# Performance work log

Measured on AMD Instinct MI355X. Metric: run time of the kernel, lower is better.

The kernel has to match this reference:

```python
import jax, jax.numpy as jnp
import numpy as np
import math

B, IMG, P, C_IN = 32, 32, 2, 4
D, TED, L, H = 768, 256, 12, 12
GRID = IMG // P            # 16
N = GRID * GRID            # 256 patches
HD = D // H                # 64 head dim
MLP_H = 4 * D
RPD = 2 * GRID - 1         # 31 relative-position table side


def _ln(x, w, b, eps=1e-6):
    m = x.mean(-1, keepdims=True)
    v = ((x - m) ** 2).mean(-1, keepdims=True)
    return (x - m) * jax.lax.rsqrt(v + eps) * w + b


def _rel_idx():
    c = jnp.arange(GRID)
    ch, cw = jnp.meshgrid(c, c, indexing='ij')
    cf = jnp.stack([ch.reshape(-1), cw.reshape(-1)])          # [2, N]
    rel = cf[:, :, None] - cf[:, None, :] + (GRID - 1)        # [2, N, N] in [0, 2*GRID-2]
    return rel[0], rel[1]


def setup_inputs() -> dict:
    key = jax.random.key(0)
    ks = iter(jax.random.split(key, 64))
    def nrm(shape, s=0.02):
        return jax.random.normal(next(ks), shape, jnp.float32) * s
    z = lambda *s: jnp.zeros(s, jnp.float32)
    o = lambda *s: jnp.ones(s, jnp.float32)
    return dict(
        x=jax.random.normal(next(ks), (B, C_IN, IMG, IMG), jnp.float32),
        t=jax.random.uniform(next(ks), (B,), jnp.float32) * 1000.0,
        patch_w=nrm((D, C_IN, P, P), 0.5), patch_b=z(D),
        pos_embed=nrm((1, N, D)),
        t_w1=nrm((TED, D)), t_b1=z(D), t_w2=nrm((D, D)), t_b2=z(D),
        norm1_w=o(L, D), norm1_b=z(L, D),
        wqs=nrm((L, D, D)), bqs=z(L, D), wqt=nrm((L, D, D)), bqt=z(L, D),
        wks=nrm((L, D, D)), bks=z(L, D), wkt=nrm((L, D, D)), bkt=z(L, D),
        wvs=nrm((L, D, D)), bvs=z(L, D), wvt=nrm((L, D, D)), bvt=z(L, D),
        attn_proj_w=nrm((L, D, D)), attn_proj_b=z(L, D),
        rpb=nrm((L, RPD, RPD, H)),
        norm2_w=o(L, D), norm2_b=z(L, D),
        mlp_w1=nrm((L, D, MLP_H)), mlp_b1=z(L, MLP_H),
        mlp_w2=nrm((L, MLP_H, D)), mlp_b2=z(L, D),
        norm_w=o(D), norm_b=z(D),
        dec_w=nrm((D, P * P * C_IN)), dec_b=z(P * P * C_IN),
    )


def reference(x, t, patch_w, patch_b, pos_embed, t_w1, t_b1, t_w2, t_b2,
              norm1_w, norm1_b, wqs, bqs, wqt, bqt, wks, bks, wkt, bkt,
              wvs, bvs, wvt, bvt, attn_proj_w, attn_proj_b, rpb,
              norm2_w, norm2_b, mlp_w1, mlp_b1, mlp_w2, mlp_b2,
              norm_w, norm_b, dec_w, dec_b):
    Bn = x.shape[0]
    # patch embed: stride==kernel Conv2d as reshape + einsum -> [B, N, D]
    xr = x.reshape(Bn, C_IN, GRID, P, GRID, P)
    x_s = jnp.einsum('bcipjq,ecpq->bije', xr, patch_w).reshape(Bn, N, D) + patch_b
    x_s = x_s + pos_embed
    # sinusoidal time embedding + MLP -> [B, D]
    half = TED // 2
    freq = jnp.exp(jnp.arange(half, dtype=jnp.float32) * (-math.log(10000.0) / (half - 1)))
    emb = t[:, None] * freq[None, :]
    emb = jnp.concatenate([jnp.sin(emb), jnp.cos(emb)], axis=-1)
    x_t = jax.nn.silu(emb @ t_w1 + t_b1) @ t_w2 + t_b2
    ih, iw = _rel_idx()
    scale = HD ** -0.5
    for l in range(L):
        h = _ln(x_s, norm1_w[l], norm1_b[l])
        q = h @ wqs[l] + bqs[l] + (x_t @ wqt[l] + bqt[l])[:, None, :]
        k = h @ wks[l] + bks[l] + (x_t @ wkt[l] + bkt[l])[:, None, :]
        v = h @ wvs[l] + bvs[l] + (x_t @ wvt[l] + bvt[l])[:, None, :]
        q = q.reshape(Bn, N, H, HD)
        k = k.reshape(Bn, N, H, HD)
        v = v.reshape(Bn, N, H, HD)
        bias = rpb[l][ih, iw]                                  # gather: [N, N, H]
        attn = jnp.einsum('bnhd,bmhd->bhnm', q, k) * scale + bias.transpose(2, 0, 1)[None]
        attn = jax.nn.softmax(attn, axis=-1)
        o_ = jnp.einsum('bhnm,bmhd->bnhd', attn, v).reshape(Bn, N, D)
        x_s = x_s + (o_ @ attn_proj_w[l] + attn_proj_b[l])
        h2 = _ln(x_s, norm2_w[l], norm2_b[l])
        x_s = x_s + (jax.nn.silu(h2 @ mlp_w1[l] + mlp_b1[l]) @ mlp_w2[l] + mlp_b2[l])
    x_s = _ln(x_s, norm_w, norm_b)
    x_s = x_s @ dec_w + dec_b                                  # [B, N, P*P*C]
    # unpatchify -> [B, C, IMG, IMG]
    xo = x_s.reshape(Bn, GRID, GRID, C_IN, P, P).transpose(0, 3, 1, 4, 2, 5)
    return xo.reshape(Bn, C_IN, GRID * P, GRID * P)
```

## Files before the change

### kernel.cpp

```cpp
#include <hip/hip_runtime.h>
#include <hip/hip_bf16.h>

typedef __attribute__((ext_vector_type(8))) short short8;
typedef __attribute__((ext_vector_type(4))) short s16x4;
typedef __attribute__((ext_vector_type(4))) float f32x4;
typedef __hip_bfloat16 bf16;

#define AS1 __attribute__((address_space(1)))
#define AS3 __attribute__((address_space(3)))

__device__ __forceinline__ float b2f(short u) {
  union { unsigned int i; float f; } x;
  x.i = ((unsigned int)(unsigned short)u) << 16;
  return x.f;
}
__device__ __forceinline__ short f2bs(float f) {
  bf16 t = __float2bfloat16(f);
  return *reinterpret_cast<short*>(&t);
}

__device__ __forceinline__ void gld_lds16(const void* g, void* lds) {
  __builtin_amdgcn_global_load_lds((const AS1 unsigned int*)g,
                                   (AS3 unsigned int*)lds, 16, 0, 0);
}

__global__ void transpose_conv(const float* __restrict__ src, bf16* __restrict__ dst,
                               int R, int C, int row_off, long long layer_stride) {
  __shared__ float t[32][33];
  int l = blockIdx.z;
  int r0 = blockIdx.y * 32;
  int c0 = blockIdx.x * 32;
  int tx = threadIdx.x & 31, ty = threadIdx.x >> 5;
  const float* s = src + (size_t)l * R * C;
#pragma unroll
  for (int i = 0; i < 4; ++i)
    t[ty + i * 8][tx] = s[(size_t)(r0 + ty + i * 8) * C + c0 + tx];
  __syncthreads();
  bf16* d = dst + (size_t)l * layer_stride;
#pragma unroll
  for (int i = 0; i < 4; ++i) {
    int n = c0 + ty + i * 8, k = r0 + tx;
    d[(size_t)(row_off + n) * R + k] = __float2bfloat16(t[tx][ty + i * 8]);
  }
}

__global__ void dec_transpose(const float* __restrict__ dw, bf16* __restrict__ dwT) {
  int idx = blockIdx.x * 256 + threadIdx.x;
  if (idx >= 12288) return;
  int k = idx % 768, j = idx / 768;
  dwT[j * 768 + k] = __float2bfloat16(dw[k * 16 + j]);
}

__global__ void patch_embed(const float* __restrict__ x, const float* __restrict__ pw,
                            const float* __restrict__ pb, const float* __restrict__ pos,
                            float* __restrict__ xs) {
  int idx = blockIdx.x * 256 + threadIdx.x;
  int d = idx % 768;
  int n = (idx / 768) & 255;
  int b = idx / (768 * 256);
  int gi = n >> 4, gj = n & 15;
  float acc = pb[d];
#pragma unroll
  for (int c = 0; c < 4; ++c)
#pragma unroll
    for (int p = 0; p < 2; ++p)
#pragma unroll
      for (int q = 0; q < 2; ++q)
        acc += x[((b * 4 + c) * 32 + gi * 2 + p) * 32 + gj * 2 + q] *
               pw[((d * 4 + c) * 2 + p) * 2 + q];
  xs[idx] = acc + pos[n * 768 + d];
}

__global__ void temb_kernel(const float* __restrict__ t, float* __restrict__ emb) {
  int b = blockIdx.x;
  int i = threadIdx.x;
  float f = __expf((float)i * (-logf(10000.f) / 127.f));
  float e = t[b] * f;
  emb[b * 256 + i] = sinf(e);
  emb[b * 256 + 128 + i] = cosf(e);
}

template <int MODE>
__global__ void smallmm_red(const float* __restrict__ in, const float* __restrict__ w,
                            const float* __restrict__ bias, void* __restrict__ out, int K) {
  int tid = threadIdx.x;
  int s = tid & 7, o = blockIdx.x * 32 + (tid >> 3);
  int d = o % 768, b = o / 768;
  int Ks = K >> 3, k0 = s * Ks;
  const float* ir = in + b * K + k0;
  const float* wr = w + (size_t)k0 * 768 + d;
  float a = 0.f;
  for (int i = 0; i < Ks; ++i) a += ir[i] * wr[(size_t)i * 768];
  a += __shfl_xor(a, 1);
  a += __shfl_xor(a, 2);
  a += __shfl_xor(a, 4);
  if (s == 0) {
    a += bias[d];
    if (MODE == 0) {
      a = a / (1.f + __expf(-a));
      ((float*)out)[o] = a;
    } else {
      ((bf16*)out)[o] = __float2bfloat16(a);
    }
  }
}

__global__ void build_btab_frag(const float* __restrict__ rpb, bf16* __restrict__ btf) {
  int idx = blockIdx.x * 256 + threadIdx.x;
  int t = idx & 65535;
  int lh = idx >> 16;
  int h = lh % 12, l = lh / 12;
  int r = t & 3; t >>= 2;
  int lane = t & 63; t >>= 6;
  int i = t & 3; t >>= 2;
  int w = t & 3; t >>= 2;
  int jb = t & 1; t >>= 1;
  int hc = t & 7;
  int q = w * 64 + i * 16 + (lane & 15);
  int k = hc * 32 + jb * 16 + (lane >> 4) * 4 + r;
  int ih = (q >> 4) - (k >> 4) + 15;
  int iw = (q & 15) - (k & 15) + 15;
  btf[idx] = __float2bfloat16(8.0f * rpb[((l * 31 + ih) * 31 + iw) * 12 + h]);
}

__global__ __launch_bounds__(256) void ln_bf16_kernel(const float* __restrict__ x,
                                                      const float* __restrict__ w,
                                                      const float* __restrict__ b,
                                                      bf16* __restrict__ out) {
  int row = blockIdx.x;
  int tid = threadIdx.x;
  const float* xr = x + (size_t)row * 768;
  float v[3];
  float s = 0.f, s2 = 0.f;
#pragma unroll
  for (int i = 0; i < 3; ++i) {
    v[i] = xr[tid + i * 256];
    s += v[i];
    s2 += v[i] * v[i];
  }
#pragma unroll
  for (int off = 32; off; off >>= 1) {
    s += __shfl_down(s, off);
    s2 += __shfl_down(s2, off);
  }
  __shared__ float ps[4], ps2[4];
  int wid = tid >> 6, lane = tid & 63;
  if (lane == 0) { ps[wid] = s; ps2[wid] = s2; }
  __syncthreads();
  s = ps[0] + ps[1] + ps[2] + ps[3];
  s2 = ps2[0] + ps2[1] + ps2[2] + ps2[3];
  float m = s * (1.f / 768.f);
  float var = s2 * (1.f / 768.f) - m * m;
  float r = rsqrtf(var + 1e-6f);
#pragma unroll
  for (int i = 0; i < 3; ++i) {
    int c = tid + i * 256;
    out[(size_t)row * 768 + c] = __float2bfloat16((v[i] - m) * r * w[c] + b[c]);
  }
}

template <int EPI>
__global__ __launch_bounds__(256) void gemm128(
    const bf16* __restrict__ A, int lda, const bf16* __restrict__ BT, int ldb, int K,
    const float* __restrict__ p0, const float* __restrict__ p1,
    const float* __restrict__ p2, const float* __restrict__ p3,
    const float* __restrict__ p4, const float* __restrict__ p5,
    const float* __restrict__ resid, float* __restrict__ outF,
    bf16* __restrict__ outB, int ldc) {
  __shared__ __align__(16) char lds[65536];
  const int tid = threadIdx.x;
  const int wid = tid >> 6, lane = tid & 63;
  const int wr = wid >> 1, wc = wid & 1;
  const int nwg = gridDim.x * gridDim.y;
  const int bid = blockIdx.y * gridDim.x + blockIdx.x;
  const int swzb = (bid & 7) * (nwg >> 3) + (bid >> 3);
  const int m0 = (swzb / gridDim.x) * 128, n0 = (swzb % gridDim.x) * 128;
  const int l16 = lane & 15, lq = lane >> 4;

  f32x4 acc[4][4];
#pragma unroll
  for (int i = 0; i < 4; ++i)
#pragma unroll
    for (int j = 0; j < 4; ++j) acc[i][j] = f32x4{0.f, 0.f, 0.f, 0.f};

  const int arow = tid >> 3;
  const int aslot = (tid & 7) ^ (arow & 7);
  const bf16* gA = A + (size_t)(m0 + arow) * lda + aslot * 8;
  const bf16* gB = BT + (size_t)(n0 + arow) * ldb + aslot * 8;
  const unsigned offw = (unsigned)__builtin_amdgcn_readfirstlane((tid & ~63) * 16);

  const int NT = K >> 6;
  auto stage = [&](int buf, int t) {
    char* p = lds + buf * 32768;
    const int k = t * 64;
#pragma unroll
    for (int it = 0; it < 4; ++it) {
      gld_lds16(gA + (size_t)it * 32 * lda + k, p + it * 4096 + offw);
      gld_lds16(gB + (size_t)it * 32 * ldb + k, p + 16384 + it * 4096 + offw);
    }
  };

  stage(0, 0);
  const unsigned swb = ((unsigned)(l16 & 7)) << 4;
  for (int t = 0; t < NT; ++t) {
    char* cur = lds + (t & 1) * 32768;
    if (t + 1 < NT) {
      stage((t + 1) & 1, t + 1);
      asm volatile("s_waitcnt vmcnt(8)" ::: "memory");
    } else {
      asm volatile("s_waitcnt vmcnt(0)" ::: "memory");
    }
    __builtin_amdgcn_s_barrier();
#pragma unroll
    for (int ks = 0; ks < 2; ++ks) {
      short8 af[4], bfr[4];
      const unsigned ko = ((unsigned)(ks * 64 + lq * 16)) ^ swb;
#pragma unroll
      for (int i = 0; i < 4; ++i) {
        af[i]  = *(const short8*)(cur + (wr * 64 + i * 16 + l16) * 128 + ko);
        bfr[i] = *(const short8*)(cur + 16384 + (wc * 64 + i * 16 + l16) * 128 + ko);
      }
#pragma unroll
      for (int i = 0; i < 4; ++i)
#pragma unroll
        for (int j = 0; j < 4; ++j)
          acc[i][j] = __builtin_amdgcn_mfma_f32_16x16x32_bf16(af[i], bfr[j], acc[i][j], 0, 0, 0);
    }
    __builtin_amdgcn_s_barrier();
  }

#pragma unroll
  for (int i = 0; i < 4; ++i) {
#pragma unroll
    for (int j = 0; j < 4; ++j) {
#pragma unroll
      for (int r = 0; r < 4; ++r) {
        int row = m0 + wr * 64 + i * 16 + lq * 4 + r;
        int col = n0 + wc * 64 + j * 16 + l16;
        float v = acc[i][j][r];
        if constexpr (EPI == 0) {
          int s = col / 768, d = col % 768;
          int b = row >> 8;
          const float* bs = (s == 0) ? p0 : (s == 1) ? p1 : p2;
          const float* ts = (s == 0) ? p3 : (s == 1) ? p4 : p5;
          v += bs[d] + ts[b * 768 + d];
          outB[(size_t)row * ldc + col] = __float2bfloat16(v);
        } else if constexpr (EPI == 1) {
          v += p0[col] + resid[(size_t)row * ldc + col];
          outF[(size_t)row * ldc + col] = v;
        } else if constexpr (EPI == 2) {
          v += p0[col];
          v = v / (1.f + __expf(-v));
          outB[(size_t)row * ldc + col] = __float2bfloat16(v);
        } else if constexpr (EPI == 3) {
          if (row < 32) {
            int l = col / 2304;
            int r2c = col - l * 2304;
            int s = r2c / 768, d = r2c - s * 768;
            const float* bs = (s == 0) ? p0 : (s == 1) ? p1 : p2;
            v += bs[l * 768 + d];
            outF[(size_t)((l * 3 + s) * 32 + row) * 768 + d] = v;
          }
        } else {
          if (col < 16) {
            v += p0[col];
            int b = row >> 8, n = row & 255;
            int gi = n >> 4, gj = n & 15;
            int c = col >> 2, pp = (col >> 1) & 1, qq = col & 1;
            outF[((b * 4 + c) * 32 + gi * 2 + pp) * 32 + gj * 2 + qq] = v;
          }
        }
      }
    }
  }
}

__global__ __launch_bounds__(256) void attn_mfma(const bf16* __restrict__ qkv,
                                                 const bf16* __restrict__ btf,
                                                 bf16* __restrict__ obuf) {
  __shared__ __align__(16) char lds[65536];
  const int tid = threadIdx.x;
  const int wave = tid >> 6, lane = tid & 63;
  const int l16 = lane & 15, lq = lane >> 4;
  const int b = blockIdx.x / 12, h = blockIdx.x % 12;
  const bf16* qb = qkv + (size_t)b * 256 * 2304;

  {
    const short8* vrow = (const short8*)(qb + (size_t)tid * 2304 + 1536 + h * 64);
    short8 vv[8];
#pragma unroll
    for (int c = 0; c < 8; ++c) vv[c] = vrow[c];
#pragma unroll
    for (int c = 0; c < 8; ++c)
#pragma unroll
      for (int e = 0; e < 8; ++e) {
        int d = c * 8 + e;
        unsigned off = (unsigned)(d * 512 + tid * 2) ^ ((unsigned)(d & 7) << 4);
        *(short*)(lds + off) = vv[c][e];
      }
  }
  short8 qf[4][2];
#pragma unroll
  for (int i = 0; i < 4; ++i)
#pragma unroll
    for (int ks = 0; ks < 2; ++ks)
      qf[i][ks] = *(const short8*)(qb + (size_t)(wave * 64 + i * 16 + l16) * 2304 +
                                   h * 64 + ks * 32 + lq * 8);
  __syncthreads();

  f32x4 oacc[4][4];
#pragma unroll
  for (int i = 0; i < 4; ++i)
#pragma unroll
    for (int j = 0; j < 4; ++j) oacc[i][j] = f32x4{0.f, 0.f, 0.f, 0.f};
  float lp[4] = {0.f, 0.f, 0.f, 0.f};
  const bf16* bl = btf + (size_t)h * 65536 + lane * 4;
  const unsigned swzv = ((unsigned)(l16 & 7)) << 4;
  const unsigned swzp = ((unsigned)(l16 & 3)) << 4;

  for (int hc = 0; hc < 8; ++hc) {
    short8 kf[2][2];
#pragma unroll
    for (int jb = 0; jb < 2; ++jb) {
      const bf16* kr = qb + (size_t)(hc * 32 + jb * 16 + l16) * 2304 + 768 + h * 64 + lq * 8;
      kf[jb][0] = *(const short8*)(kr);
      kf[jb][1] = *(const short8*)(kr + 32);
    }
    f32x4 sacc[4][2];
#pragma unroll
    for (int i = 0; i < 4; ++i)
#pragma unroll
      for (int jb = 0; jb < 2; ++jb) {
        s16x4 bv = *(const s16x4*)(bl + ((size_t)((hc * 2 + jb) * 16 + wave * 4 + i) << 8));
        sacc[i][jb] = f32x4{b2f(bv[0]), b2f(bv[1]), b2f(bv[2]), b2f(bv[3])};
      }
#pragma unroll
    for (int jb = 0; jb < 2; ++jb)
#pragma unroll
      for (int i = 0; i < 4; ++i) {
        sacc[i][jb] = __builtin_amdgcn_mfma_f32_16x16x32_bf16(kf[jb][0], qf[i][0], sacc[i][jb], 0, 0, 0);
        sacc[i][jb] = __builtin_amdgcn_mfma_f32_16x16x32_bf16(kf[jb][1], qf[i][1], sacc[i][jb], 0, 0, 0);
      }
    char* Pw = lds + 32768 + (hc & 1) * 16384 + wave * 4096;
#pragma unroll
    for (int i = 0; i < 4; ++i)
#pragma unroll
      for (int jb = 0; jb < 2; ++jb) {
        float p0 = __expf(sacc[i][jb][0] * 0.125f);
        float p1 = __expf(sacc[i][jb][1] * 0.125f);
        float p2 = __expf(sacc[i][jb][2] * 0.125f);
        float p3 = __expf(sacc[i][jb][3] * 0.125f);
        lp[i] += (p0 + p1) + (p2 + p3);
        s16x4 pk = {f2bs(p0), f2bs(p1), f2bs(p2), f2bs(p3)};
        *(s16x4*)(Pw + (i * 16 + l16) * 64 + (((unsigned)(jb * 32 + lq * 8)) ^ swzp)) = pk;
      }
    asm volatile("s_waitcnt lgkmcnt(0)" ::: "memory");
    __builtin_amdgcn_sched_barrier(0);
    short8 pa[4], vb[4];
#pragma unroll
    for (int i = 0; i < 4; ++i)
      pa[i] = *(const short8*)(Pw + (i * 16 + l16) * 64 + (((unsigned)(lq * 16)) ^ swzp));
#pragma unroll
    for (int dj = 0; dj < 4; ++dj)
      vb[dj] = *(const short8*)(lds + (dj * 16 + l16) * 512 +
                                (((unsigned)(hc * 64 + lq * 16)) ^ swzv));
#pragma unroll
    for (int i = 0; i < 4; ++i)
#pragma unroll
      for (int dj = 0; dj < 4; ++dj)
        oacc[i][dj] = __builtin_amdgcn_mfma_f32_16x16x32_bf16(pa[i], vb[dj], oacc[i][dj], 0, 0, 0);
  }

#pragma unroll
  for (int i = 0; i < 4; ++i) {
    float l = lp[i];
    l += __shfl_xor(l, 16);
    l += __shfl_xor(l, 32);
#pragma unroll
    for (int r = 0; r < 4; ++r) {
      float linv = 1.f / __shfl(l, lq * 4 + r);
      int grow = b * 256 + wave * 64 + i * 16 + lq * 4 + r;
#pragma unroll
      for (int dj = 0; dj < 4; ++dj)
        obuf[(size_t)grow * 768 + h * 64 + dj * 16 + l16] =
            __float2bfloat16(oacc[i][dj][r] * linv);
    }
  }
}

extern "C" void kernel_launch(void* const* d_in, const int* in_sizes, int n_in,
                              void* d_out, int out_size, void* d_ws, size_t ws_size,
                              hipStream_t stream) {
  (void)in_sizes; (void)n_in; (void)out_size; (void)ws_size;
  const float* x       = (const float*)d_in[0];
  const float* t_in    = (const float*)d_in[1];
  const float* patch_w = (const float*)d_in[2];
  const float* patch_b = (const float*)d_in[3];
  const float* pos     = (const float*)d_in[4];
  const float* t_w1    = (const float*)d_in[5];
  const float* t_b1    = (const float*)d_in[6];
  const float* t_w2    = (const float*)d_in[7];
  const float* t_b2    = (const float*)d_in[8];
  const float* norm1_w = (const float*)d_in[9];
  const float* norm1_b = (const float*)d_in[10];
  const float* wqs     = (const float*)d_in[11];
  const float* bqs     = (const float*)d_in[12];
  const float* wqt     = (const float*)d_in[13];
  const float* bqt     = (const float*)d_in[14];
  const float* wks     = (const float*)d_in[15];
  const float* bks     = (const float*)d_in[16];
  const float* wkt     = (const float*)d_in[17];
  const float* bkt     = (const float*)d_in[18];
  const float* wvs     = (const float*)d_in[19];
  const float* bvs     = (const float*)d_in[20];
  const float* wvt     = (const float*)d_in[21];
  const float* bvt     = (const float*)d_in[22];
  const float* projw   = (const float*)d_in[23];
  const float* projb   = (const float*)d_in[24];
  const float* rpb     = (const float*)d_in[25];
  const float* norm2_w = (const float*)d_in[26];
  const float* norm2_b = (const float*)d_in[27];
  const float* mlp_w1  = (const float*)d_in[28];
  const float* mlp_b1  = (const float*)d_in[29];
  const float* mlp_w2  = (const float*)d_in[30];
  const float* mlp_b2  = (const float*)d_in[31];
  const float* norm_w  = (const float*)d_in[32];
  const float* norm_b  = (const float*)d_in[33];
  const float* dec_w   = (const float*)d_in[34];
  const float* dec_b   = (const float*)d_in[35];

  char* ws = (char*)d_ws;
  size_t off = 0;
  auto alloc = [&](size_t bytes) -> void* {
    void* p = ws + off;
    off += (bytes + 255) & ~(size_t)255;
    return p;
  };
  bf16* wqkvT = (bf16*)alloc(12ull * 2304 * 768 * 2);
  bf16* projT = (bf16*)alloc(12ull * 768 * 768 * 2);
  bf16* mlp1T = (bf16*)alloc(12ull * 3072 * 768 * 2);
  bf16* mlp2T = (bf16*)alloc(12ull * 768 * 3072 * 2);
  bf16* wtT   = (bf16*)alloc(12ull * 2304 * 768 * 2);
  float* xs   = (float*)alloc(8192ull * 768 * 4);
  bf16* hbuf  = (bf16*)alloc(8192ull * 768 * 2);
  bf16* qkvb  = (bf16*)alloc(8192ull * 2304 * 2);
  bf16* obuf  = (bf16*)alloc(8192ull * 768 * 2);
  bf16* btabf = (bf16*)alloc(12ull * 12 * 256 * 256 * 2);
  float* ttok = (float*)alloc(12ull * 3 * 32 * 768 * 4);
  bf16* xtb   = (bf16*)alloc(128ull * 768 * 2);
  bf16* dwT   = (bf16*)alloc(128ull * 768 * 2);
  float* emb  = (float*)alloc(32ull * 256 * 4);
  float* h1   = (float*)alloc(32ull * 768 * 4);
  bf16* hmlp  = qkvb;

  hipMemsetAsync(xtb, 0, 128ull * 768 * 2, stream);
  hipMemsetAsync(dwT, 0, 128ull * 768 * 2, stream);

  transpose_conv<<<dim3(24, 24, 12), 256, 0, stream>>>(wqs, wqkvT, 768, 768, 0, 2304ll * 768);
  transpose_conv<<<dim3(24, 24, 12), 256, 0, stream>>>(wks, wqkvT, 768, 768, 768, 2304ll * 768);
  transpose_conv<<<dim3(24, 24, 12), 256, 0, stream>>>(wvs, wqkvT, 768, 768, 1536, 2304ll * 768);
  transpose_conv<<<dim3(24, 24, 12), 256, 0, stream>>>(projw, projT, 768, 768, 0, 768ll * 768);
  transpose_conv<<<dim3(96, 24, 12), 256, 0, stream>>>(mlp_w1, mlp1T, 768, 3072, 0, 3072ll * 768);
  transpose_conv<<<dim3(24, 96, 12), 256, 0, stream>>>(mlp_w2, mlp2T, 3072, 768, 0, 768ll * 3072);
  transpose_conv<<<dim3(24, 24, 12), 256, 0, stream>>>(wqt, wtT, 768, 768, 0, 2304ll * 768);
  transpose_conv<<<dim3(24, 24, 12), 256, 0, stream>>>(wkt, wtT, 768, 768, 768, 2304ll * 768);
  transpose_conv<<<dim3(24, 24, 12), 256, 0, stream>>>(wvt, wtT, 768, 768, 1536, 2304ll * 768);
  dec_transpose<<<48, 256, 0, stream>>>(dec_w, dwT);
  build_btab_frag<<<36864, 256, 0, stream>>>(rpb, btabf);

  temb_kernel<<<32, 128, 0, stream>>>(t_in, emb);
  smallmm_red<0><<<768, 256, 0, stream>>>(emb, t_w1, t_b1, h1, 256);
  smallmm_red<1><<<768, 256, 0, stream>>>(h1, t_w2, t_b2, xtb, 768);
  gemm128<3><<<dim3(216, 1), 256, 0, stream>>>(
      xtb, 768, wtT, 768, 768, bqt, bkt, bvt, nullptr, nullptr, nullptr,
      nullptr, ttok, nullptr, 0);

  patch_embed<<<24576, 256, 0, stream>>>(x, patch_w, patch_b, pos, xs);

  for (int l = 0; l < 12; ++l) {
    ln_bf16_kernel<<<8192, 256, 0, stream>>>(xs, norm1_w + l * 768, norm1_b + l * 768, hbuf);
    gemm128<0><<<dim3(18, 64), 256, 0, stream>>>(
        hbuf, 768, wqkvT + (size_t)l * 2304 * 768, 768, 768,
        bqs + l * 768, bks + l * 768, bvs + l * 768,
        ttok + (size_t)(l * 3 + 0) * 32 * 768,
        ttok + (size_t)(l * 3 + 1) * 32 * 768,
        ttok + (size_t)(l * 3 + 2) * 32 * 768,
        nullptr, nullptr, qkvb, 2304);
    attn_mfma<<<384, 256, 0, stream>>>(qkvb, btabf + (size_t)l * 12 * 65536, obuf);
    gemm128<1><<<dim3(6, 64), 256, 0, stream>>>(
        obuf, 768, projT + (size_t)l * 768 * 768, 768, 768,
        projb + l * 768, nullptr, nullptr, nullptr, nullptr, nullptr,
        xs, xs, nullptr, 768);
    ln_bf16_kernel<<<8192, 256, 0, stream>>>(xs, norm2_w + l * 768, norm2_b + l * 768, hbuf);
    gemm128<2><<<dim3(24, 64), 256, 0, stream>>>(
        hbuf, 768, mlp1T + (size_t)l * 3072 * 768, 768, 768,
        mlp_b1 + l * 3072, nullptr, nullptr, nullptr, nullptr, nullptr,
        nullptr, nullptr, hmlp, 3072);
    gemm128<1><<<dim3(6, 64), 256, 0, stream>>>(
        hmlp, 3072, mlp2T + (size_t)l * 768 * 3072, 3072, 3072,
        mlp_b2 + l * 768, nullptr, nullptr, nullptr, nullptr, nullptr,
        xs, xs, nullptr, 768);
  }
  ln_bf16_kernel<<<8192, 256, 0, stream>>>(xs, norm_w, norm_b, hbuf);
  gemm128<4><<<dim3(1, 64), 256, 0, stream>>>(
      hbuf, 768, dwT, 768, 768, dec_b, nullptr, nullptr, nullptr, nullptr, nullptr,
      nullptr, (float*)d_out, nullptr, 0);
}
```

Baseline: 2.841 ms.

## Replace 128x128 GEMM with 256x128 tile, 8 waves, quadrant-phased pipeline

The GEMM tile grows from 128x128 with 4 waves to 256x128 with 8 waves, and LDS rises to 96 KB. The K-loop is split into four quadrant phases, each of which issues part of the next stages' global-to-LDS loads before its MFMA burst. MFMA runs are wrapped in raised s_setprio, and the block swizzle is made conditional on the grid size. The aim is more reuse of A/B per tile and better overlap of loads with MFMA, at the cost of one workgroup per CU and fewer workgroups for the narrow N=768 GEMMs. The xtb buffer is enlarged so the timestep GEMM can read 256 rows.

After: 3.314 ms. 16.6% more time.

```diff
diff --git a/kernel.cpp b/kernel.cpp
--- a/kernel.cpp
+++ b/kernel.cpp
@@ -159,23 +159,59 @@
   }
 }
 
+#define ENDB do { __builtin_amdgcn_sched_barrier(0); __builtin_amdgcn_s_barrier(); \
+                  __builtin_amdgcn_sched_barrier(0); } while (0)
+
+#define PH(MQ, NQ, STG) do {                                                         \
+    char* pa = lds + ((t & 1) << 15) + (MQ << 14);                                   \
+    char* pb = lds + 65536 + ((t & 1) << 14) + (NQ << 13);                           \
+    short8 af0, af1, af2, af3, bg0, bg1, bg2, bg3;                                   \
+    {                                                                                \
+      int ra0 = wm * 32 + l16, ra1 = ra0 + 16;                                       \
+      unsigned sa0 = (unsigned)(ra0 & 7) << 4, sa1 = (unsigned)(ra1 & 7) << 4;       \
+      af0 = *(const short8*)(pa + ra0 * 128 + (((unsigned)(lq * 16)) ^ sa0));        \
+      af1 = *(const short8*)(pa + ra0 * 128 + (((unsigned)(64 + lq * 16)) ^ sa0));   \
+      af2 = *(const short8*)(pa + ra1 * 128 + (((unsigned)(lq * 16)) ^ sa1));        \
+      af3 = *(const short8*)(pa + ra1 * 128 + (((unsigned)(64 + lq * 16)) ^ sa1));   \
+      int rb0 = wn * 32 + l16, rb1 = rb0 + 16;                                       \
+      unsigned sb0 = (unsigned)(rb0 & 7) << 4, sb1 = (unsigned)(rb1 & 7) << 4;       \
+      bg0 = *(const short8*)(pb + rb0 * 128 + (((unsigned)(lq * 16)) ^ sb0));        \
+      bg1 = *(const short8*)(pb + rb0 * 128 + (((unsigned)(64 + lq * 16)) ^ sb0));   \
+      bg2 = *(const short8*)(pb + rb1 * 128 + (((unsigned)(lq * 16)) ^ sb1));        \
+      bg3 = *(const short8*)(pb + rb1 * 128 + (((unsigned)(64 + lq * 16)) ^ sb1));   \
+    }                                                                                \
+    STG;                                                                             \
+    ENDB;                                                                            \
+    __builtin_amdgcn_s_setprio(1);                                                   \
+    acc[MQ*2+0][NQ*2+0] = __builtin_amdgcn_mfma_f32_16x16x32_bf16(af0, bg0, acc[MQ*2+0][NQ*2+0], 0, 0, 0); \
+    acc[MQ*2+0][NQ*2+0] = __builtin_amdgcn_mfma_f32_16x16x32_bf16(af1, bg1, acc[MQ*2+0][NQ*2+0], 0, 0, 0); \
+    acc[MQ*2+0][NQ*2+1] = __builtin_amdgcn_mfma_f32_16x16x32_bf16(af0, bg2, acc[MQ*2+0][NQ*2+1], 0, 0, 0); \
+    acc[MQ*2+0][NQ*2+1] = __builtin_amdgcn_mfma_f32_16x16x32_bf16(af1, bg3, acc[MQ*2+0][NQ*2+1], 0, 0, 0); \
+    acc[MQ*2+1][NQ*2+0] = __builtin_amdgcn_mfma_f32_16x16x32_bf16(af2, bg0, acc[MQ*2+1][NQ*2+0], 0, 0, 0); \
+    acc[MQ*2+1][NQ*2+0] = __builtin_amdgcn_mfma_f32_16x16x32_bf16(af3, bg1, acc[MQ*2+1][NQ*2+0], 0, 0, 0); \
+    acc[MQ*2+1][NQ*2+1] = __builtin_amdgcn_mfma_f32_16x16x32_bf16(af2, bg2, acc[MQ*2+1][NQ*2+1], 0, 0, 0); \
+    acc[MQ*2+1][NQ*2+1] = __builtin_amdgcn_mfma_f32_16x16x32_bf16(af3, bg3, acc[MQ*2+1][NQ*2+1], 0, 0, 0); \
+    __builtin_amdgcn_s_setprio(0);                                                   \
+  } while (0)
+
 template <int EPI>
-__global__ __launch_bounds__(256) void gemm128(
+__global__ __launch_bounds__(512, 1) void gemm256(
     const bf16* __restrict__ A, int lda, const bf16* __restrict__ BT, int ldb, int K,
     const float* __restrict__ p0, const float* __restrict__ p1,
     const float* __restrict__ p2, const float* __restrict__ p3,
     const float* __restrict__ p4, const float* __restrict__ p5,
     const float* __restrict__ resid, float* __restrict__ outF,
     bf16* __restrict__ outB, int ldc) {
-  __shared__ __align__(16) char lds[65536];
+  __shared__ __align__(16) char lds[98304];
   const int tid = threadIdx.x;
   const int wid = tid >> 6, lane = tid & 63;
-  const int wr = wid >> 1, wc = wid & 1;
+  const int wm = wid >> 1, wn = wid & 1;
+  const int l16 = lane & 15, lq = lane >> 4;
+
   const int nwg = gridDim.x * gridDim.y;
-  const int bid = blockIdx.y * gridDim.x + blockIdx.x;
-  const int swzb = (bid & 7) * (nwg >> 3) + (bid >> 3);
-  const int m0 = (swzb / gridDim.x) * 128, n0 = (swzb % gridDim.x) * 128;
-  const int l16 = lane & 15, lq = lane >> 4;
+  int bid = blockIdx.y * gridDim.x + blockIdx.x;
+  if (!(nwg & 7)) bid = (bid & 7) * (nwg >> 3) + (bid >> 3);
+  const int m0 = (bid / gridDim.x) * 256, n0 = (bid % gridDim.x) * 128;
 
   f32x4 acc[4][4];
 #pragma unroll
@@ -183,50 +219,44 @@
 #pragma unroll
     for (int j = 0; j < 4; ++j) acc[i][j] = f32x4{0.f, 0.f, 0.f, 0.f};
 
-  const int arow = tid >> 3;
-  const int aslot = (tid & 7) ^ (arow & 7);
-  const bf16* gA = A + (size_t)(m0 + arow) * lda + aslot * 8;
-  const bf16* gB = BT + (size_t)(n0 + arow) * ldb + aslot * 8;
+  const int u5 = (tid >> 3) & 31;
+  const int slot = (tid & 7) ^ ((tid >> 3) & 7);
+  const bf16* gA = A + (size_t)m0 * lda + slot * 8;
+  const bf16* gB = BT + (size_t)n0 * ldb + slot * 8;
   const unsigned offw = (unsigned)__builtin_amdgcn_readfirstlane((tid & ~63) * 16);
 
-  const int NT = K >> 6;
-  auto stage = [&](int buf, int t) {
-    char* p = lds + buf * 32768;
-    const int k = t * 64;
-#pragma unroll
-    for (int it = 0; it < 4; ++it) {
-      gld_lds16(gA + (size_t)it * 32 * lda + k, p + it * 4096 + offw);
-      gld_lds16(gB + (size_t)it * 32 * ldb + k, p + 16384 + it * 4096 + offw);
+  auto stageA = [&](int tt, int mq) {
+    char* dst = lds + ((tt & 1) << 15) + (mq << 14);
+#pragma unroll
+    for (int e = 0; e < 2; ++e) {
+      int srow = (e * 2 + (tid >> 8)) * 64 + mq * 32 + u5;
+      gld_lds16(gA + (size_t)srow * lda + tt * 64, dst + e * 8192 + offw);
     }
   };
-
-  stage(0, 0);
-  const unsigned swb = ((unsigned)(l16 & 7)) << 4;
+  auto stageB = [&](int tt, int nq) {
+    char* dst = lds + 65536 + ((tt & 1) << 14) + (nq << 13);
+    int srow = ((tid >> 8) & 1) * 64 + nq * 32 + u5;
+    gld_lds16(gB + (size_t)srow * ldb + tt * 64, dst + offw);
+  };
+
+  const int NT = K >> 6;
+  stageA(0, 0); stageA(0, 1); stageB(0, 0); stageB(0, 1);
+  stageB(1, 0); stageA(1, 0);
+  asm volatile("s_waitcnt vmcnt(3)" ::: "memory");
+  __builtin_amdgcn_s_barrier();
+  __builtin_amdgcn_sched_barrier(0);
+
   for (int t = 0; t < NT; ++t) {
-    char* cur = lds + (t & 1) * 32768;
-    if (t + 1 < NT) {
-      stage((t + 1) & 1, t + 1);
-      asm volatile("s_waitcnt vmcnt(8)" ::: "memory");
-    } else {
-      asm volatile("s_waitcnt vmcnt(0)" ::: "memory");
-    }
-    __builtin_amdgcn_s_barrier();
-#pragma unroll
-    for (int ks = 0; ks < 2; ++ks) {
-      short8 af[4], bfr[4];
-      const unsigned ko = ((unsigned)(ks * 64 + lq * 16)) ^ swb;
-#pragma unroll
-      for (int i = 0; i < 4; ++i) {
-        af[i]  = *(const short8*)(cur + (wr * 64 + i * 16 + l16) * 128 + ko);
-        bfr[i] = *(const short8*)(cur + 16384 + (wc * 64 + i * 16 + l16) * 128 + ko);
-      }
-#pragma unroll
-      for (int i = 0; i < 4; ++i)
-#pragma unroll
-        for (int j = 0; j < 4; ++j)
-          acc[i][j] = __builtin_amdgcn_mfma_f32_16x16x32_bf16(af[i], bfr[j], acc[i][j], 0, 0, 0);
-    }
-    __builtin_amdgcn_s_barrier();
+    PH(0, 0, { if (t + 1 < NT) stageA(t + 1, 1); });
+    ENDB;
+    PH(1, 0, { if (t + 1 < NT) stageB(t + 1, 1); });
+    ENDB;
+    PH(0, 1, { if (t + 2 < NT) stageB(t + 2, 0); });
+    ENDB;
+    PH(1, 1, { if (t + 2 < NT) stageA(t + 2, 0); });
+    if (t + 2 < NT) { asm volatile("s_waitcnt vmcnt(3)" ::: "memory"); }
+    else            { asm volatile("s_waitcnt vmcnt(0)" ::: "memory"); }
+    ENDB;
   }
 
 #pragma unroll
@@ -235,8 +265,8 @@
     for (int j = 0; j < 4; ++j) {
 #pragma unroll
       for (int r = 0; r < 4; ++r) {
-        int row = m0 + wr * 64 + i * 16 + lq * 4 + r;
-        int col = n0 + wc * 64 + j * 16 + l16;
+        int row = m0 + wm * 64 + (i >> 1) * 32 + (i & 1) * 16 + lq * 4 + r;
+        int col = n0 + wn * 64 + (j >> 1) * 32 + (j & 1) * 16 + l16;
         float v = acc[i][j][r];
         if constexpr (EPI == 0) {
           int s = col / 768, d = col % 768;
@@ -447,13 +477,13 @@
   bf16* obuf  = (bf16*)alloc(8192ull * 768 * 2);
   bf16* btabf = (bf16*)alloc(12ull * 12 * 256 * 256 * 2);
   float* ttok = (float*)alloc(12ull * 3 * 32 * 768 * 4);
-  bf16* xtb   = (bf16*)alloc(128ull * 768 * 2);
+  bf16* xtb   = (bf16*)alloc(256ull * 768 * 2);
   bf16* dwT   = (bf16*)alloc(128ull * 768 * 2);
   float* emb  = (float*)alloc(32ull * 256 * 4);
   float* h1   = (float*)alloc(32ull * 768 * 4);
   bf16* hmlp  = qkvb;
 
-  hipMemsetAsync(xtb, 0, 128ull * 768 * 2, stream);
+  hipMemsetAsync(xtb, 0, 256ull * 768 * 2, stream);
   hipMemsetAsync(dwT, 0, 128ull * 768 * 2, stream);
 
   transpose_conv<<<dim3(24, 24, 12), 256, 0, stream>>>(wqs, wqkvT, 768, 768, 0, 2304ll * 768);
@@ -471,7 +501,7 @@
   temb_kernel<<<32, 128, 0, stream>>>(t_in, emb);
   smallmm_red<0><<<768, 256, 0, stream>>>(emb, t_w1, t_b1, h1, 256);
   smallmm_red<1><<<768, 256, 0, stream>>>(h1, t_w2, t_b2, xtb, 768);
-  gemm128<3><<<dim3(216, 1), 256, 0, stream>>>(
+  gemm256<3><<<dim3(216, 1), 512, 0, stream>>>(
       xtb, 768, wtT, 768, 768, bqt, bkt, bvt, nullptr, nullptr, nullptr,
       nullptr, ttok, nullptr, 0);
 
@@ -479,7 +509,7 @@
 
   for (int l = 0; l < 12; ++l) {
     ln_bf16_kernel<<<8192, 256, 0, stream>>>(xs, norm1_w + l * 768, norm1_b + l * 768, hbuf);
-    gemm128<0><<<dim3(18, 64), 256, 0, stream>>>(
+    gemm256<0><<<dim3(18, 32), 512, 0, stream>>>(
         hbuf, 768, wqkvT + (size_t)l * 2304 * 768, 768, 768,
         bqs + l * 768, bks + l * 768, bvs + l * 768,
         ttok + (size_t)(l * 3 + 0) * 32 * 768,
@@ -487,22 +517,22 @@
         ttok + (size_t)(l * 3 + 2) * 32 * 768,
         nullptr, nullptr, qkvb, 2304);
     attn_mfma<<<384, 256, 0, stream>>>(qkvb, btabf + (size_t)l * 12 * 65536, obuf);
-    gemm128<1><<<dim3(6, 64), 256, 0, stream>>>(
+    gemm256<1><<<dim3(6, 32), 512, 0, stream>>>(
         obuf, 768, projT + (size_t)l * 768 * 768, 768, 768,
         projb + l * 768, nullptr, nullptr, nullptr, nullptr, nullptr,
         xs, xs, nullptr, 768);
     ln_bf16_kernel<<<8192, 256, 0, stream>>>(xs, norm2_w + l * 768, norm2_b + l * 768, hbuf);
-    gemm128<2><<<dim3(24, 64), 256, 0, stream>>>(
+    gemm256<2><<<dim3(24, 32), 512, 0, stream>>>(
         hbuf, 768, mlp1T + (size_t)l * 3072 * 768, 768, 768,
         mlp_b1 + l * 3072, nullptr, nullptr, nullptr, nullptr, nullptr,
         nullptr, nullptr, hmlp, 3072);
-    gemm128<1><<<dim3(6, 64), 256, 0, stream>>>(
+    gemm256<1><<<dim3(6, 32), 512, 0, stream>>>(
         hmlp, 3072, mlp2T + (size_t)l * 768 * 3072, 3072, 3072,
         mlp_b2 + l * 768, nullptr, nullptr, nullptr, nullptr, nullptr,
         xs, xs, nullptr, 768);
   }
   ln_bf16_kernel<<<8192, 256, 0, stream>>>(xs, norm_w, norm_b, hbuf);
-  gemm128<4><<<dim3(1, 64), 256, 0, stream>>>(
+  gemm256<4><<<dim3(1, 32), 512, 0, stream>>>(
       hbuf, 768, dwT, 768, 768, dec_b, nullptr, nullptr, nullptr, nullptr, nullptr,
       nullptr, (float*)d_out, nullptr, 0);
 }
```

## Halve GEMM K-tile to cut LDS use; make LayerNorm one wave per row

Applied to the files above, without the earlier changes.

The GEMM K-tile shrinks from 64 to 32, so LDS per block drops from 64KB to 32KB. The load mapping, swizzle and vmcnt waits are reworked to match. The aim is to fit more workgroups per CU for latency hiding, at the cost of twice as many barriers and waits per K step. LayerNorm now assigns one wavefront per row with an xor-shuffle reduction, which drops the LDS exchange and __syncthreads and launches a quarter as many blocks.

New measurement: 3.041 ms. 7.0% more time.

```diff
diff --git a/kernel.cpp b/kernel.cpp
--- a/kernel.cpp
+++ b/kernel.cpp
@@ -127,35 +127,30 @@
                                                       const float* __restrict__ w,
                                                       const float* __restrict__ b,
                                                       bf16* __restrict__ out) {
-  int row = blockIdx.x;
-  int tid = threadIdx.x;
+  int row = blockIdx.x * 4 + (threadIdx.x >> 6);
+  int lane = threadIdx.x & 63;
   const float* xr = x + (size_t)row * 768;
-  float v[3];
+  float v[12];
   float s = 0.f, s2 = 0.f;
 #pragma unroll
-  for (int i = 0; i < 3; ++i) {
-    v[i] = xr[tid + i * 256];
-    s += v[i];
-    s2 += v[i] * v[i];
+  for (int k = 0; k < 12; ++k) {
+    v[k] = xr[lane + k * 64];
+    s += v[k];
+    s2 += v[k] * v[k];
   }
 #pragma unroll
   for (int off = 32; off; off >>= 1) {
-    s += __shfl_down(s, off);
-    s2 += __shfl_down(s2, off);
-  }
-  __shared__ float ps[4], ps2[4];
-  int wid = tid >> 6, lane = tid & 63;
-  if (lane == 0) { ps[wid] = s; ps2[wid] = s2; }
-  __syncthreads();
-  s = ps[0] + ps[1] + ps[2] + ps[3];
-  s2 = ps2[0] + ps2[1] + ps2[2] + ps2[3];
+    s += __shfl_xor(s, off);
+    s2 += __shfl_xor(s2, off);
+  }
   float m = s * (1.f / 768.f);
   float var = s2 * (1.f / 768.f) - m * m;
   float r = rsqrtf(var + 1e-6f);
-#pragma unroll
-  for (int i = 0; i < 3; ++i) {
-    int c = tid + i * 256;
-    out[(size_t)row * 768 + c] = __float2bfloat16((v[i] - m) * r * w[c] + b[c]);
+  bf16* orow = out + (size_t)row * 768;
+#pragma unroll
+  for (int k = 0; k < 12; ++k) {
+    int c = lane + k * 64;
+    orow[c] = __float2bfloat16((v[k] - m) * r * w[c] + b[c]);
   }
 }
 
@@ -167,7 +162,7 @@
     const float* __restrict__ p4, const float* __restrict__ p5,
     const float* __restrict__ resid, float* __restrict__ outF,
     bf16* __restrict__ outB, int ldc) {
-  __shared__ __align__(16) char lds[65536];
+  __shared__ __align__(16) char lds[32768];
   const int tid = threadIdx.x;
   const int wid = tid >> 6, lane = tid & 63;
   const int wr = wid >> 1, wc = wid & 1;
@@ -183,49 +178,48 @@
 #pragma unroll
     for (int j = 0; j < 4; ++j) acc[i][j] = f32x4{0.f, 0.f, 0.f, 0.f};
 
-  const int arow = tid >> 3;
-  const int aslot = (tid & 7) ^ (arow & 7);
+  const int arow = tid >> 2;
+  const int aslot = (tid & 3) ^ (arow & 3);
   const bf16* gA = A + (size_t)(m0 + arow) * lda + aslot * 8;
   const bf16* gB = BT + (size_t)(n0 + arow) * ldb + aslot * 8;
   const unsigned offw = (unsigned)__builtin_amdgcn_readfirstlane((tid & ~63) * 16);
 
-  const int NT = K >> 6;
-  auto stage = [&](int buf, int t) {
-    char* p = lds + buf * 32768;
-    const int k = t * 64;
-#pragma unroll
-    for (int it = 0; it < 4; ++it) {
-      gld_lds16(gA + (size_t)it * 32 * lda + k, p + it * 4096 + offw);
-      gld_lds16(gB + (size_t)it * 32 * ldb + k, p + 16384 + it * 4096 + offw);
+  const int NT = K >> 5;
+  auto stage = [&](int t) {
+    char* pA = lds + (t & 1) * 8192;
+    char* pB = lds + 16384 + (t & 1) * 8192;
+    const int k = t * 32;
+#pragma unroll
+    for (int e = 0; e < 2; ++e) {
+      gld_lds16(gA + (size_t)(e * 64) * lda + k, pA + e * 4096 + offw);
+      gld_lds16(gB + (size_t)(e * 64) * ldb + k, pB + e * 4096 + offw);
     }
   };
 
-  stage(0, 0);
-  const unsigned swb = ((unsigned)(l16 & 7)) << 4;
+  stage(0);
   for (int t = 0; t < NT; ++t) {
-    char* cur = lds + (t & 1) * 32768;
+    char* pA = lds + (t & 1) * 8192;
+    char* pB = lds + 16384 + (t & 1) * 8192;
     if (t + 1 < NT) {
-      stage((t + 1) & 1, t + 1);
-      asm volatile("s_waitcnt vmcnt(8)" ::: "memory");
+      stage(t + 1);
+      asm volatile("s_waitcnt vmcnt(4)" ::: "memory");
     } else {
       asm volatile("s_waitcnt vmcnt(0)" ::: "memory");
     }
     __builtin_amdgcn_s_barrier();
-#pragma unroll
-    for (int ks = 0; ks < 2; ++ks) {
-      short8 af[4], bfr[4];
-      const unsigned ko = ((unsigned)(ks * 64 + lq * 16)) ^ swb;
-#pragma unroll
-      for (int i = 0; i < 4; ++i) {
-        af[i]  = *(const short8*)(cur + (wr * 64 + i * 16 + l16) * 128 + ko);
-        bfr[i] = *(const short8*)(cur + 16384 + (wc * 64 + i * 16 + l16) * 128 + ko);
-      }
-#pragma unroll
-      for (int i = 0; i < 4; ++i)
-#pragma unroll
-        for (int j = 0; j < 4; ++j)
-          acc[i][j] = __builtin_amdgcn_mfma_f32_16x16x32_bf16(af[i], bfr[j], acc[i][j], 0, 0, 0);
-    }
+    short8 af[4], bfr[4];
+    const unsigned sw = ((unsigned)(l16 & 3)) << 4;
+    const unsigned ko = ((unsigned)(lq * 16)) ^ sw;
+#pragma unroll
+    for (int i = 0; i < 4; ++i) {
+      af[i]  = *(const short8*)(pA + (wr * 64 + i * 16 + l16) * 64 + ko);
+      bfr[i] = *(const short8*)(pB + (wc * 64 + i * 16 + l16) * 64 + ko);
+    }
+#pragma unroll
+    for (int i = 0; i < 4; ++i)
+#pragma unroll
+      for (int j = 0; j < 4; ++j)
+        acc[i][j] = __builtin_amdgcn_mfma_f32_16x16x32_bf16(af[i], bfr[j], acc[i][j], 0, 0, 0);
     __builtin_amdgcn_s_barrier();
   }
 
@@ -478,7 +472,7 @@
   patch_embed<<<24576, 256, 0, stream>>>(x, patch_w, patch_b, pos, xs);
 
   for (int l = 0; l < 12; ++l) {
-    ln_bf16_kernel<<<8192, 256, 0, stream>>>(xs, norm1_w + l * 768, norm1_b + l * 768, hbuf);
+    ln_bf16_kernel<<<2048, 256, 0, stream>>>(xs, norm1_w + l * 768, norm1_b + l * 768, hbuf);
     gemm128<0><<<dim3(18, 64), 256, 0, stream>>>(
         hbuf, 768, wqkvT + (size_t)l * 2304 * 768, 768, 768,
         bqs + l * 768, bks + l * 768, bvs + l * 768,
@@ -491,7 +485,7 @@
         obuf, 768, projT + (size_t)l * 768 * 768, 768, 768,
         projb + l * 768, nullptr, nullptr, nullptr, nullptr, nullptr,
         xs, xs, nullptr, 768);
-    ln_bf16_kernel<<<8192, 256, 0, stream>>>(xs, norm2_w + l * 768, norm2_b + l * 768, hbuf);
+    ln_bf16_kernel<<<2048, 256, 0, stream>>>(xs, norm2_w + l * 768, norm2_b + l * 768, hbuf);
     gemm128<2><<<dim3(24, 64), 256, 0, stream>>>(
         hbuf, 768, mlp1T + (size_t)l * 3072 * 768, 768, 768,
         mlp_b1 + l * 3072, nullptr, nullptr, nullptr, nullptr, nullptr,
@@ -501,7 +495,7 @@
         mlp_b2 + l * 768, nullptr, nullptr, nullptr, nullptr, nullptr,
         xs, xs, nullptr, 768);
   }
-  ln_bf16_kernel<<<8192, 256, 0, stream>>>(xs, norm_w, norm_b, hbuf);
+  ln_bf16_kernel<<<2048, 256, 0, stream>>>(xs, norm_w, norm_b, hbuf);
   gemm128<4><<<dim3(1, 64), 256, 0, stream>>>(
       hbuf, 768, dwT, 768, 768, dec_b, nullptr, nullptr, nullptr, nullptr, nullptr,
       nullptr, (float*)d_out, nullptr, 0);
```
